# Kernel optimization log

Measured on AMD Instinct MI355X. Metric: run time of the kernel, lower is better.

The kernel has to match this reference:

```python
import jax, jax.numpy as jnp
import numpy as np

IN_CH = 10
OUT_CH = 11
EPS = 1e-5  # torch LayerNorm default


def setup_inputs() -> dict:
    key = jax.random.key(0)
    k_x, k_w = jax.random.split(key, 2)
    N = 8192
    x = jax.random.normal(k_x, (N, IN_CH), dtype=jnp.float32)
    # torch nn.Linear weight: [out_features=3*OUT_CH, in_features=IN_CH]
    W = jax.random.normal(k_w, (3 * OUT_CH, IN_CH), dtype=jnp.float32) * (IN_CH ** -0.5)
    gamma = jnp.ones((IN_CH,), dtype=jnp.float32)
    beta = jnp.zeros((IN_CH,), dtype=jnp.float32)
    return {"x": x, "gamma": gamma, "beta": beta, "W": W}


def reference(x, gamma, beta, W):
    # LayerNorm over channel dim
    mu = jnp.mean(x, axis=-1, keepdims=True)
    var = jnp.var(x, axis=-1, keepdims=True)
    h = (x - mu) / jnp.sqrt(var + EPS) * gamma + beta  # [N, IN_CH]
    # Linear (no bias): x @ W.T -> [N, 3*OUT_CH]
    h = h @ W.T
    # chunk along dim=1 (channel dim for 2D input)
    q, k, v = jnp.split(h, 3, axis=1)  # each [N, OUT_CH]
    scale = IN_CH ** -0.5  # note: scale uses in_channels, per source
    q = q * scale
    sim = jnp.einsum('id,jd->ij', q, k)  # [N, N]
    sim = sim - jax.lax.stop_gradient(jnp.max(sim, axis=-1, keepdims=True))
    attn = jax.nn.softmax(sim, axis=-1)
    out = jnp.einsum('ij,jd->id', attn, v)  # [N, OUT_CH]
    return out
```

## Files before the change

### kernel.cpp

```cpp
#include <hip/hip_runtime.h>

#define NROWS 8192
#define INCH 10
#define NQKV 33
#define OUTCH 11
#define SPLIT 16
#define KB 512
#define QBLK 128

typedef short short8 __attribute__((ext_vector_type(8)));
typedef float f32x16 __attribute__((ext_vector_type(16)));
typedef unsigned int uvec4 __attribute__((ext_vector_type(4)));

#define QB_OFF   0
#define KB_OFF   (NROWS * 32)
#define VT_OFF   (2 * NROWS * 32)
#define PART_OFF (3 * NROWS * 32)

#define SWAP32(a, b) asm("v_permlane32_swap_b32 %0, %1" : "+v"(a), "+v"(b))

__device__ inline unsigned short f2bf(float f) {
  unsigned u = __float_as_uint(f);
  unsigned r = (u + 0x7FFFu + ((u >> 16) & 1u)) >> 16;
  return (unsigned short)r;
}

__global__ __launch_bounds__(128) void qkv_ln_kernel(
    const float* __restrict__ x, const float* __restrict__ gamma,
    const float* __restrict__ beta, const float* __restrict__ W,
    char* __restrict__ ws) {
  __shared__ float sW[NQKV * INCH];
  __shared__ float sg[INCH];
  __shared__ float sb[INCH];
  int tid = threadIdx.x;
  for (int i = tid; i < NQKV * INCH; i += 128) sW[i] = W[i];
  if (tid < INCH) { sg[tid] = gamma[tid]; sb[tid] = beta[tid]; }
  __syncthreads();

  int row = blockIdx.x * 128 + tid;
  const float2* x2 = (const float2*)x;
  float xv[INCH];
#pragma unroll
  for (int j = 0; j < 5; ++j) {
    float2 t = x2[row * 5 + j];
    xv[2 * j] = t.x;
    xv[2 * j + 1] = t.y;
  }

  float mu = 0.f;
#pragma unroll
  for (int i = 0; i < INCH; ++i) mu += xv[i];
  mu *= (1.0f / INCH);
  float var = 0.f;
#pragma unroll
  for (int i = 0; i < INCH; ++i) { float d = xv[i] - mu; var += d * d; }
  var *= (1.0f / INCH);
  float rstd = rsqrtf(var + 1e-5f);
  float h[INCH];
#pragma unroll
  for (int i = 0; i < INCH; ++i) h[i] = (xv[i] - mu) * rstd * sg[i] + sb[i];

  float acc[NQKV];
#pragma unroll
  for (int oc = 0; oc < NQKV; ++oc) {
    float s = 0.f;
#pragma unroll
    for (int i = 0; i < INCH; ++i) s += h[i] * sW[oc * INCH + i];
    acc[oc] = s;
  }

  const float QSC = 0.31622776601683794f * 1.4426950408889634f;

  unsigned short e[16];
  unsigned qw[8];
#pragma unroll
  for (int i = 0; i < 16; ++i) e[i] = (i < OUTCH) ? f2bf(acc[i] * QSC) : 0;
#pragma unroll
  for (int i = 0; i < 8; ++i)
    qw[i] = (unsigned)e[2 * i] | ((unsigned)e[2 * i + 1] << 16);
  uint4* Qb = (uint4*)(ws + QB_OFF);
  Qb[row * 2 + 0] = make_uint4(qw[0], qw[1], qw[2], qw[3]);
  Qb[row * 2 + 1] = make_uint4(qw[4], qw[5], qw[6], qw[7]);
#pragma unroll
  for (int i = 0; i < 16; ++i) e[i] = (i < OUTCH) ? f2bf(acc[OUTCH + i]) : 0;
#pragma unroll
  for (int i = 0; i < 8; ++i)
    qw[i] = (unsigned)e[2 * i] | ((unsigned)e[2 * i + 1] << 16);
  uint4* Kb = (uint4*)(ws + KB_OFF);
  Kb[row * 2 + 0] = make_uint4(qw[0], qw[1], qw[2], qw[3]);
  Kb[row * 2 + 1] = make_uint4(qw[4], qw[5], qw[6], qw[7]);
  unsigned short* VTu = (unsigned short*)(ws + VT_OFF);
  int u0 = (row >> 3) * 16;
  int slot = row & 7;
#pragma unroll
  for (int d = 0; d < 16; ++d) {
    unsigned short v;
    if (d < OUTCH)       v = f2bf(acc[2 * OUTCH + d]);
    else if (d == OUTCH) v = 0x3F80;
    else                 v = 0;
    VTu[(u0 + d) * 8 + slot] = v;
  }
}

__global__ __launch_bounds__(256) void attn_kernel(const char* __restrict__ ws,
                                                   float* __restrict__ part) {
  __shared__ uint4 sK[KB * 2];
  __shared__ uint4 sVT[KB * 2];

  const int tid = threadIdx.x;
  const int lane = tid & 63;
  const int wv = tid >> 6;
  const int h = lane >> 5;
  const int l31 = lane & 31;
  const int qc = blockIdx.x >> 4;
  const int kc = blockIdx.x & 15;
  const int kt0 = kc * KB;
  const int q0 = qc * QBLK + wv * 32;

  const uint4* Qb = (const uint4*)(ws + QB_OFF);
  const uint4* gK = (const uint4*)(ws + KB_OFF) + kt0 * 2;
  const uint4* gV = (const uint4*)(ws + VT_OFF) + kt0 * 2;

#pragma unroll
  for (int i = 0; i < 4; ++i) {
    int o = wv * 64 + 256 * i;
    __builtin_amdgcn_global_load_lds(
        (const __attribute__((address_space(1))) void*)(gK + o + lane),
        (__attribute__((address_space(3))) void*)(sK + o), 16, 0, 0);
    __builtin_amdgcn_global_load_lds(
        (const __attribute__((address_space(1))) void*)(gV + o + lane),
        (__attribute__((address_space(3))) void*)(sVT + o), 16, 0, 0);
  }

  short8 qf = *(const short8*)((const char*)Qb + (q0 + l31) * 32 + h * 16);

  f32x16 oacc;
#pragma unroll
  for (int r = 0; r < 16; ++r) oacc[r] = 0.f;
  f32x16 zf;
#pragma unroll
  for (int r = 0; r < 16; ++r) zf[r] = 0.f;

  __syncthreads();

  for (int it = 0; it < KB / 32; ++it) {
    short8 kf = *(const short8*)((const char*)sK + it * 1024 + l31 * 32 + h * 16);
    f32x16 s = __builtin_amdgcn_mfma_f32_32x32x16_bf16(kf, qf, zf, 0, 0, 0);

    float p[16];
#pragma unroll
    for (int r = 0; r < 16; ++r) p[r] = __builtin_amdgcn_exp2f(s[r]);

#define PK(a, b) __builtin_amdgcn_perm(__float_as_uint(b), __float_as_uint(a), 0x07060302u)
    unsigned P01 = PK(p[0], p[1]), P23 = PK(p[2], p[3]);
    unsigned P45 = PK(p[4], p[5]), P67 = PK(p[6], p[7]);
    unsigned P89 = PK(p[8], p[9]), Pab = PK(p[10], p[11]);
    unsigned Pcd = PK(p[12], p[13]), Pef = PK(p[14], p[15]);
#undef PK
    SWAP32(P01, P45);
    SWAP32(P23, P67);
    SWAP32(P89, Pcd);
    SWAP32(Pab, Pef);

    uvec4 c0 = {P01, P23, P45, P67};
    uvec4 c1 = {P89, Pab, Pcd, Pef};
    short8 a0 = __builtin_bit_cast(short8, c0);
    short8 a1 = __builtin_bit_cast(short8, c1);

    const char* vb = (const char*)sVT;
    short8 v0 = *(const short8*)(vb + (it * 4 + h) * 256 + (lane & 15) * 16);
    short8 v1 = *(const short8*)(vb + (it * 4 + 2 + h) * 256 + (lane & 15) * 16);

    oacc = __builtin_amdgcn_mfma_f32_32x32x16_bf16(a0, v0, oacc, 0, 0, 0);
    oacc = __builtin_amdgcn_mfma_f32_32x32x16_bf16(a1, v1, oacc, 0, 0, 0);
  }

  if (l31 < 12) {
#pragma unroll
    for (int r = 0; r < 16; ++r) {
      int q = (r & 3) + 8 * (r >> 2) + 4 * h;
      part[((size_t)kc * NROWS + q0 + q) * 12 + l31] = oacc[r];
    }
  }
}

__global__ __launch_bounds__(128) void norm_kernel(const float* __restrict__ part,
                                                   float* __restrict__ out) {
  int row = blockIdx.x * 128 + threadIdx.x;
  const float4* p4 = (const float4*)part;
  float r[12];
#pragma unroll
  for (int d = 0; d < 12; ++d) r[d] = 0.f;
#pragma unroll
  for (int kc = 0; kc < SPLIT; ++kc) {
    size_t b = ((size_t)kc * NROWS + row) * 3;
    float4 t0 = p4[b], t1 = p4[b + 1], t2 = p4[b + 2];
    r[0] += t0.x; r[1] += t0.y; r[2] += t0.z; r[3] += t0.w;
    r[4] += t1.x; r[5] += t1.y; r[6] += t1.z; r[7] += t1.w;
    r[8] += t2.x; r[9] += t2.y; r[10] += t2.z; r[11] += t2.w;
  }
  float inv = 1.0f / r[11];
  float* o = out + (size_t)row * OUTCH;
#pragma unroll
  for (int d = 0; d < OUTCH; ++d) o[d] = r[d] * inv;
}

extern "C" void kernel_launch(void* const* d_in, const int* in_sizes, int n_in,
                              void* d_out, int out_size, void* d_ws, size_t ws_size,
                              hipStream_t stream) {
  const float* x = (const float*)d_in[0];
  const float* gamma = (const float*)d_in[1];
  const float* beta = (const float*)d_in[2];
  const float* W = (const float*)d_in[3];
  char* ws = (char*)d_ws;
  float* out = (float*)d_out;
  float* part = (float*)(ws + PART_OFF);

  qkv_ln_kernel<<<NROWS / 128, 128, 0, stream>>>(x, gamma, beta, W, ws);
  attn_kernel<<<(NROWS / QBLK) * SPLIT, 256, 0, stream>>>(ws, part);
  norm_kernel<<<NROWS / 128, 128, 0, stream>>>(part, out);
}
```

Baseline: 25.91 us.

## Process two query tiles per wave to reuse K loads and split K layout

Each wave now handles 64 query rows (two 32-row MFMA tiles) against the same K fragment, doubling QBLK to 256 and halving the attention grid. K is stored as two planar halves (first and second 16 bytes of each row separately), so LDS reads of K become contiguous per half-wave. The pre- and post-processing kernels move to 64-thread blocks, giving more blocks. The intent is to amortize K/V LDS reads and staging across more queries and add MFMA-level ILP, at the cost of more registers and fewer attention blocks (512 instead of 1024), which may reduce occupancy or load balance.

Result: slower. 27.77 us (+7.2%).

```diff
diff --git a/kernel.cpp b/kernel.cpp
--- a/kernel.cpp
+++ b/kernel.cpp
@@ -6,7 +6,7 @@
 #define OUTCH 11
 #define SPLIT 16
 #define KB 512
-#define QBLK 128
+#define QBLK 256
 
 typedef short short8 __attribute__((ext_vector_type(8)));
 typedef float f32x16 __attribute__((ext_vector_type(16)));
@@ -25,7 +25,7 @@
   return (unsigned short)r;
 }
 
-__global__ __launch_bounds__(128) void qkv_ln_kernel(
+__global__ __launch_bounds__(64) void qkv_ln_kernel(
     const float* __restrict__ x, const float* __restrict__ gamma,
     const float* __restrict__ beta, const float* __restrict__ W,
     char* __restrict__ ws) {
@@ -33,11 +33,11 @@
   __shared__ float sg[INCH];
   __shared__ float sb[INCH];
   int tid = threadIdx.x;
-  for (int i = tid; i < NQKV * INCH; i += 128) sW[i] = W[i];
+  for (int i = tid; i < NQKV * INCH; i += 64) sW[i] = W[i];
   if (tid < INCH) { sg[tid] = gamma[tid]; sb[tid] = beta[tid]; }
   __syncthreads();
 
-  int row = blockIdx.x * 128 + tid;
+  int row = blockIdx.x * 64 + tid;
   const float2* x2 = (const float2*)x;
   float xv[INCH];
 #pragma unroll
@@ -87,8 +87,8 @@
   for (int i = 0; i < 8; ++i)
     qw[i] = (unsigned)e[2 * i] | ((unsigned)e[2 * i + 1] << 16);
   uint4* Kb = (uint4*)(ws + KB_OFF);
-  Kb[row * 2 + 0] = make_uint4(qw[0], qw[1], qw[2], qw[3]);
-  Kb[row * 2 + 1] = make_uint4(qw[4], qw[5], qw[6], qw[7]);
+  Kb[row] = make_uint4(qw[0], qw[1], qw[2], qw[3]);
+  Kb[NROWS + row] = make_uint4(qw[4], qw[5], qw[6], qw[7]);
   unsigned short* VTu = (unsigned short*)(ws + VT_OFF);
   int u0 = (row >> 3) * 16;
   int slot = row & 7;
@@ -104,7 +104,7 @@
 
 __global__ __launch_bounds__(256) void attn_kernel(const char* __restrict__ ws,
                                                    float* __restrict__ part) {
-  __shared__ uint4 sK[KB * 2];
+  __shared__ uint4 sK[2 * KB];
   __shared__ uint4 sVT[KB * 2];
 
   const int tid = threadIdx.x;
@@ -115,78 +115,94 @@
   const int qc = blockIdx.x >> 4;
   const int kc = blockIdx.x & 15;
   const int kt0 = kc * KB;
-  const int q0 = qc * QBLK + wv * 32;
-
-  const uint4* Qb = (const uint4*)(ws + QB_OFF);
-  const uint4* gK = (const uint4*)(ws + KB_OFF) + kt0 * 2;
+  const int q0 = qc * QBLK + wv * 64;
+
+  const uint4* gK = (const uint4*)(ws + KB_OFF);
   const uint4* gV = (const uint4*)(ws + VT_OFF) + kt0 * 2;
 
+#pragma unroll
+  for (int c = 0; c < 2; ++c) {
+#pragma unroll
+    for (int i = 0; i < 2; ++i) {
+      int o = wv * 64 + 256 * i;
+      __builtin_amdgcn_global_load_lds(
+          (const __attribute__((address_space(1))) void*)(gK + c * NROWS + kt0 + o + lane),
+          (__attribute__((address_space(3))) void*)(sK + c * KB + o), 16, 0, 0);
+    }
+  }
 #pragma unroll
   for (int i = 0; i < 4; ++i) {
     int o = wv * 64 + 256 * i;
     __builtin_amdgcn_global_load_lds(
-        (const __attribute__((address_space(1))) void*)(gK + o + lane),
-        (__attribute__((address_space(3))) void*)(sK + o), 16, 0, 0);
-    __builtin_amdgcn_global_load_lds(
         (const __attribute__((address_space(1))) void*)(gV + o + lane),
         (__attribute__((address_space(3))) void*)(sVT + o), 16, 0, 0);
   }
 
-  short8 qf = *(const short8*)((const char*)Qb + (q0 + l31) * 32 + h * 16);
-
-  f32x16 oacc;
-#pragma unroll
-  for (int r = 0; r < 16; ++r) oacc[r] = 0.f;
-  f32x16 zf;
-#pragma unroll
-  for (int r = 0; r < 16; ++r) zf[r] = 0.f;
+  const char* Qb = ws + QB_OFF;
+  short8 qf0 = *(const short8*)(Qb + (q0 + l31) * 32 + h * 16);
+  short8 qf1 = *(const short8*)(Qb + (q0 + 32 + l31) * 32 + h * 16);
+
+  f32x16 oacc0, oacc1, zf;
+#pragma unroll
+  for (int r = 0; r < 16; ++r) { oacc0[r] = 0.f; oacc1[r] = 0.f; zf[r] = 0.f; }
 
   __syncthreads();
 
   for (int it = 0; it < KB / 32; ++it) {
-    short8 kf = *(const short8*)((const char*)sK + it * 1024 + l31 * 32 + h * 16);
-    f32x16 s = __builtin_amdgcn_mfma_f32_32x32x16_bf16(kf, qf, zf, 0, 0, 0);
-
-    float p[16];
-#pragma unroll
-    for (int r = 0; r < 16; ++r) p[r] = __builtin_amdgcn_exp2f(s[r]);
-
-#define PK(a, b) __builtin_amdgcn_perm(__float_as_uint(b), __float_as_uint(a), 0x07060302u)
-    unsigned P01 = PK(p[0], p[1]), P23 = PK(p[2], p[3]);
-    unsigned P45 = PK(p[4], p[5]), P67 = PK(p[6], p[7]);
-    unsigned P89 = PK(p[8], p[9]), Pab = PK(p[10], p[11]);
-    unsigned Pcd = PK(p[12], p[13]), Pef = PK(p[14], p[15]);
-#undef PK
-    SWAP32(P01, P45);
-    SWAP32(P23, P67);
-    SWAP32(P89, Pcd);
-    SWAP32(Pab, Pef);
-
-    uvec4 c0 = {P01, P23, P45, P67};
-    uvec4 c1 = {P89, Pab, Pcd, Pef};
-    short8 a0 = __builtin_bit_cast(short8, c0);
-    short8 a1 = __builtin_bit_cast(short8, c1);
+    short8 kf = *(const short8*)((const char*)sK + h * (KB * 16) +
+                                 (it * 32 + l31) * 16);
+    f32x16 s0 = __builtin_amdgcn_mfma_f32_32x32x16_bf16(kf, qf0, zf, 0, 0, 0);
+    f32x16 s1 = __builtin_amdgcn_mfma_f32_32x32x16_bf16(kf, qf1, zf, 0, 0, 0);
 
     const char* vb = (const char*)sVT;
     short8 v0 = *(const short8*)(vb + (it * 4 + h) * 256 + (lane & 15) * 16);
     short8 v1 = *(const short8*)(vb + (it * 4 + 2 + h) * 256 + (lane & 15) * 16);
 
-    oacc = __builtin_amdgcn_mfma_f32_32x32x16_bf16(a0, v0, oacc, 0, 0, 0);
-    oacc = __builtin_amdgcn_mfma_f32_32x32x16_bf16(a1, v1, oacc, 0, 0, 0);
+#define PK(a, b) __builtin_amdgcn_perm(__float_as_uint(b), __float_as_uint(a), 0x07060302u)
+#define MKFRAG(sv, A0, A1)                                                   \
+  {                                                                          \
+    float p[16];                                                             \
+    _Pragma("unroll") for (int r = 0; r < 16; ++r)                           \
+        p[r] = __builtin_amdgcn_exp2f(sv[r]);                                \
+    unsigned P01 = PK(p[0], p[1]), P23 = PK(p[2], p[3]);                     \
+    unsigned P45 = PK(p[4], p[5]), P67 = PK(p[6], p[7]);                     \
+    unsigned P89 = PK(p[8], p[9]), Pab = PK(p[10], p[11]);                   \
+    unsigned Pcd = PK(p[12], p[13]), Pef = PK(p[14], p[15]);                 \
+    SWAP32(P01, P45);                                                        \
+    SWAP32(P23, P67);                                                        \
+    SWAP32(P89, Pcd);                                                        \
+    SWAP32(Pab, Pef);                                                        \
+    uvec4 c0 = {P01, P23, P45, P67};                                         \
+    uvec4 c1 = {P89, Pab, Pcd, Pef};                                         \
+    A0 = __builtin_bit_cast(short8, c0);                                     \
+    A1 = __builtin_bit_cast(short8, c1);                                     \
+  }
+
+    short8 a00, a01, a10, a11;
+    MKFRAG(s0, a00, a01)
+    MKFRAG(s1, a10, a11)
+#undef MKFRAG
+#undef PK
+
+    oacc0 = __builtin_amdgcn_mfma_f32_32x32x16_bf16(a00, v0, oacc0, 0, 0, 0);
+    oacc0 = __builtin_amdgcn_mfma_f32_32x32x16_bf16(a01, v1, oacc0, 0, 0, 0);
+    oacc1 = __builtin_amdgcn_mfma_f32_32x32x16_bf16(a10, v0, oacc1, 0, 0, 0);
+    oacc1 = __builtin_amdgcn_mfma_f32_32x32x16_bf16(a11, v1, oacc1, 0, 0, 0);
   }
 
   if (l31 < 12) {
 #pragma unroll
     for (int r = 0; r < 16; ++r) {
       int q = (r & 3) + 8 * (r >> 2) + 4 * h;
-      part[((size_t)kc * NROWS + q0 + q) * 12 + l31] = oacc[r];
+      part[((size_t)kc * NROWS + q0 + q) * 12 + l31] = oacc0[r];
+      part[((size_t)kc * NROWS + q0 + 32 + q) * 12 + l31] = oacc1[r];
     }
   }
 }
 
-__global__ __launch_bounds__(128) void norm_kernel(const float* __restrict__ part,
-                                                   float* __restrict__ out) {
-  int row = blockIdx.x * 128 + threadIdx.x;
+__global__ __launch_bounds__(64) void norm_kernel(const float* __restrict__ part,
+                                                  float* __restrict__ out) {
+  int row = blockIdx.x * 64 + threadIdx.x;
   const float4* p4 = (const float4*)part;
   float r[12];
 #pragma unroll
@@ -216,7 +232,7 @@
   float* out = (float*)d_out;
   float* part = (float*)(ws + PART_OFF);
 
-  qkv_ln_kernel<<<NROWS / 128, 128, 0, stream>>>(x, gamma, beta, W, ws);
+  qkv_ln_kernel<<<NROWS / 64, 64, 0, stream>>>(x, gamma, beta, W, ws);
   attn_kernel<<<(NROWS / QBLK) * SPLIT, 256, 0, stream>>>(ws, part);
-  norm_kernel<<<NROWS / 128, 128, 0, stream>>>(part, out);
-}
+  norm_kernel<<<NROWS / 64, 64, 0, stream>>>(part, out);
+}
```

## Fuse LayerNorm and QKV projection into attention kernel, recomputing K/V per block

Applied to the files above, without the earlier changes.

Removes the separate QKV/LayerNorm kernel. Each attention block now recomputes LayerNorm and the projection for its 512 key rows and 128 query rows and writes K, V-transposed and Q straight into shared memory. This saves one kernel launch and the global round trip for Q/K/V. In exchange there is redundant work: K/V for each key chunk are recomputed by all 64 query blocks, and the layout of K in shared memory changes. The norm kernel block size also drops to 64 threads.

Measured after the change: 31.89 us. +23.1%, slower.

```diff
diff --git a/kernel.cpp b/kernel.cpp
--- a/kernel.cpp
+++ b/kernel.cpp
@@ -12,10 +12,6 @@
 typedef float f32x16 __attribute__((ext_vector_type(16)));
 typedef unsigned int uvec4 __attribute__((ext_vector_type(4)));
 
-#define QB_OFF   0
-#define KB_OFF   (NROWS * 32)
-#define VT_OFF   (2 * NROWS * 32)
-#define PART_OFF (3 * NROWS * 32)
 
 #define SWAP32(a, b) asm("v_permlane32_swap_b32 %0, %1" : "+v"(a), "+v"(b))
 
@@ -25,87 +21,16 @@
   return (unsigned short)r;
 }
 
-__global__ __launch_bounds__(128) void qkv_ln_kernel(
+__global__ __launch_bounds__(256) void fused_attn_kernel(
     const float* __restrict__ x, const float* __restrict__ gamma,
     const float* __restrict__ beta, const float* __restrict__ W,
-    char* __restrict__ ws) {
+    float* __restrict__ part) {
+  __shared__ uint4 sK[2 * KB];
+  __shared__ uint4 sVT[(KB / 8) * 16];
+  __shared__ uint4 sQ[QBLK * 2];
   __shared__ float sW[NQKV * INCH];
   __shared__ float sg[INCH];
   __shared__ float sb[INCH];
-  int tid = threadIdx.x;
-  for (int i = tid; i < NQKV * INCH; i += 128) sW[i] = W[i];
-  if (tid < INCH) { sg[tid] = gamma[tid]; sb[tid] = beta[tid]; }
-  __syncthreads();
-
-  int row = blockIdx.x * 128 + tid;
-  const float2* x2 = (const float2*)x;
-  float xv[INCH];
-#pragma unroll
-  for (int j = 0; j < 5; ++j) {
-    float2 t = x2[row * 5 + j];
-    xv[2 * j] = t.x;
-    xv[2 * j + 1] = t.y;
-  }
-
-  float mu = 0.f;
-#pragma unroll
-  for (int i = 0; i < INCH; ++i) mu += xv[i];
-  mu *= (1.0f / INCH);
-  float var = 0.f;
-#pragma unroll
-  for (int i = 0; i < INCH; ++i) { float d = xv[i] - mu; var += d * d; }
-  var *= (1.0f / INCH);
-  float rstd = rsqrtf(var + 1e-5f);
-  float h[INCH];
-#pragma unroll
-  for (int i = 0; i < INCH; ++i) h[i] = (xv[i] - mu) * rstd * sg[i] + sb[i];
-
-  float acc[NQKV];
-#pragma unroll
-  for (int oc = 0; oc < NQKV; ++oc) {
-    float s = 0.f;
-#pragma unroll
-    for (int i = 0; i < INCH; ++i) s += h[i] * sW[oc * INCH + i];
-    acc[oc] = s;
-  }
-
-  const float QSC = 0.31622776601683794f * 1.4426950408889634f;
-
-  unsigned short e[16];
-  unsigned qw[8];
-#pragma unroll
-  for (int i = 0; i < 16; ++i) e[i] = (i < OUTCH) ? f2bf(acc[i] * QSC) : 0;
-#pragma unroll
-  for (int i = 0; i < 8; ++i)
-    qw[i] = (unsigned)e[2 * i] | ((unsigned)e[2 * i + 1] << 16);
-  uint4* Qb = (uint4*)(ws + QB_OFF);
-  Qb[row * 2 + 0] = make_uint4(qw[0], qw[1], qw[2], qw[3]);
-  Qb[row * 2 + 1] = make_uint4(qw[4], qw[5], qw[6], qw[7]);
-#pragma unroll
-  for (int i = 0; i < 16; ++i) e[i] = (i < OUTCH) ? f2bf(acc[OUTCH + i]) : 0;
-#pragma unroll
-  for (int i = 0; i < 8; ++i)
-    qw[i] = (unsigned)e[2 * i] | ((unsigned)e[2 * i + 1] << 16);
-  uint4* Kb = (uint4*)(ws + KB_OFF);
-  Kb[row * 2 + 0] = make_uint4(qw[0], qw[1], qw[2], qw[3]);
-  Kb[row * 2 + 1] = make_uint4(qw[4], qw[5], qw[6], qw[7]);
-  unsigned short* VTu = (unsigned short*)(ws + VT_OFF);
-  int u0 = (row >> 3) * 16;
-  int slot = row & 7;
-#pragma unroll
-  for (int d = 0; d < 16; ++d) {
-    unsigned short v;
-    if (d < OUTCH)       v = f2bf(acc[2 * OUTCH + d]);
-    else if (d == OUTCH) v = 0x3F80;
-    else                 v = 0;
-    VTu[(u0 + d) * 8 + slot] = v;
-  }
-}
-
-__global__ __launch_bounds__(256) void attn_kernel(const char* __restrict__ ws,
-                                                   float* __restrict__ part) {
-  __shared__ uint4 sK[KB * 2];
-  __shared__ uint4 sVT[KB * 2];
 
   const int tid = threadIdx.x;
   const int lane = tid & 63;
@@ -115,36 +40,107 @@
   const int qc = blockIdx.x >> 4;
   const int kc = blockIdx.x & 15;
   const int kt0 = kc * KB;
-  const int q0 = qc * QBLK + wv * 32;
-
-  const uint4* Qb = (const uint4*)(ws + QB_OFF);
-  const uint4* gK = (const uint4*)(ws + KB_OFF) + kt0 * 2;
-  const uint4* gV = (const uint4*)(ws + VT_OFF) + kt0 * 2;
-
-#pragma unroll
-  for (int i = 0; i < 4; ++i) {
-    int o = wv * 64 + 256 * i;
-    __builtin_amdgcn_global_load_lds(
-        (const __attribute__((address_space(1))) void*)(gK + o + lane),
-        (__attribute__((address_space(3))) void*)(sK + o), 16, 0, 0);
-    __builtin_amdgcn_global_load_lds(
-        (const __attribute__((address_space(1))) void*)(gV + o + lane),
-        (__attribute__((address_space(3))) void*)(sVT + o), 16, 0, 0);
-  }
-
-  short8 qf = *(const short8*)((const char*)Qb + (q0 + l31) * 32 + h * 16);
-
-  f32x16 oacc;
-#pragma unroll
-  for (int r = 0; r < 16; ++r) oacc[r] = 0.f;
-  f32x16 zf;
-#pragma unroll
-  for (int r = 0; r < 16; ++r) zf[r] = 0.f;
-
+  const int q0blk = qc * QBLK;
+  const int q0 = q0blk + wv * 32;
+
+  for (int i = tid; i < NQKV * INCH; i += 256) sW[i] = W[i];
+  if (tid < INCH) { sg[tid] = gamma[tid]; sb[tid] = beta[tid]; }
   __syncthreads();
 
+  const float2* x2 = (const float2*)x;
+  const float QSC = 0.31622776601683794f * 1.4426950408889634f;
+
+#define LNROW(row, hh)                                                     \
+  {                                                                        \
+    float xv[INCH];                                                        \
+    _Pragma("unroll") for (int j = 0; j < 5; ++j) {                        \
+      float2 t = x2[(row) * 5 + j];                                        \
+      xv[2 * j] = t.x;                                                     \
+      xv[2 * j + 1] = t.y;                                                 \
+    }                                                                      \
+    float mu = 0.f;                                                        \
+    _Pragma("unroll") for (int i = 0; i < INCH; ++i) mu += xv[i];          \
+    mu *= (1.0f / INCH);                                                   \
+    float var = 0.f;                                                       \
+    _Pragma("unroll") for (int i = 0; i < INCH; ++i) {                     \
+      float d = xv[i] - mu;                                                \
+      var += d * d;                                                        \
+    }                                                                      \
+    var *= (1.0f / INCH);                                                  \
+    float rstd = rsqrtf(var + 1e-5f);                                      \
+    _Pragma("unroll") for (int i = 0; i < INCH; ++i)                       \
+        hh[i] = (xv[i] - mu) * rstd * sg[i] + sb[i];                       \
+  }
+
+#pragma unroll
+  for (int i = 0; i < 2; ++i) {
+    int r = tid + 256 * i;
+    int row = kt0 + r;
+    float hv[INCH];
+    LNROW(row, hv)
+    float acc[NQKV - OUTCH];
+#pragma unroll
+    for (int oc = 0; oc < NQKV - OUTCH; ++oc) {
+      float s = 0.f;
+#pragma unroll
+      for (int j = 0; j < INCH; ++j) s += hv[j] * sW[(OUTCH + oc) * INCH + j];
+      acc[oc] = s;
+    }
+    unsigned short e[16];
+#pragma unroll
+    for (int j = 0; j < 16; ++j) e[j] = (j < OUTCH) ? f2bf(acc[j]) : 0;
+    unsigned qw[8];
+#pragma unroll
+    for (int j = 0; j < 8; ++j)
+      qw[j] = (unsigned)e[2 * j] | ((unsigned)e[2 * j + 1] << 16);
+    sK[r] = uint4{qw[0], qw[1], qw[2], qw[3]};
+    sK[KB + r] = uint4{qw[4], qw[5], qw[6], qw[7]};
+    unsigned short* vtu = (unsigned short*)sVT;
+    int u0 = (r >> 3) * 16;
+    int slot = r & 7;
+#pragma unroll
+    for (int d = 0; d < 16; ++d) {
+      unsigned short v;
+      if (d < OUTCH)       v = f2bf(acc[OUTCH + d]);
+      else if (d == OUTCH) v = 0x3F80;
+      else                 v = 0;
+      vtu[(u0 + d) * 8 + slot] = v;
+    }
+  }
+  if (tid < QBLK) {
+    int row = q0blk + tid;
+    float hv[INCH];
+    LNROW(row, hv)
+    unsigned short e[16];
+#pragma unroll
+    for (int oc = 0; oc < 16; ++oc) {
+      float s = 0.f;
+      if (oc < OUTCH) {
+#pragma unroll
+        for (int j = 0; j < INCH; ++j) s += hv[j] * sW[oc * INCH + j];
+      }
+      e[oc] = (oc < OUTCH) ? f2bf(s * QSC) : 0;
+    }
+    unsigned qw[8];
+#pragma unroll
+    for (int j = 0; j < 8; ++j)
+      qw[j] = (unsigned)e[2 * j] | ((unsigned)e[2 * j + 1] << 16);
+    sQ[tid * 2 + 0] = uint4{qw[0], qw[1], qw[2], qw[3]};
+    sQ[tid * 2 + 1] = uint4{qw[4], qw[5], qw[6], qw[7]};
+  }
+#undef LNROW
+
+  __syncthreads();
+
+  short8 qf = *(const short8*)((const char*)sQ + (wv * 32 + l31) * 32 + h * 16);
+
+  f32x16 oacc, zf;
+#pragma unroll
+  for (int r = 0; r < 16; ++r) { oacc[r] = 0.f; zf[r] = 0.f; }
+
   for (int it = 0; it < KB / 32; ++it) {
-    short8 kf = *(const short8*)((const char*)sK + it * 1024 + l31 * 32 + h * 16);
+    short8 kf = *(const short8*)((const char*)sK + h * (KB * 16) +
+                                 (it * 32 + l31) * 16);
     f32x16 s = __builtin_amdgcn_mfma_f32_32x32x16_bf16(kf, qf, zf, 0, 0, 0);
 
     float p[16];
@@ -161,7 +157,6 @@
     SWAP32(P23, P67);
     SWAP32(P89, Pcd);
     SWAP32(Pab, Pef);
-
     uvec4 c0 = {P01, P23, P45, P67};
     uvec4 c1 = {P89, Pab, Pcd, Pef};
     short8 a0 = __builtin_bit_cast(short8, c0);
@@ -184,9 +179,9 @@
   }
 }
 
-__global__ __launch_bounds__(128) void norm_kernel(const float* __restrict__ part,
-                                                   float* __restrict__ out) {
-  int row = blockIdx.x * 128 + threadIdx.x;
+__global__ __launch_bounds__(64) void norm_kernel(const float* __restrict__ part,
+                                                  float* __restrict__ out) {
+  int row = blockIdx.x * 64 + threadIdx.x;
   const float4* p4 = (const float4*)part;
   float r[12];
 #pragma unroll
@@ -212,11 +207,10 @@
   const float* gamma = (const float*)d_in[1];
   const float* beta = (const float*)d_in[2];
   const float* W = (const float*)d_in[3];
-  char* ws = (char*)d_ws;
+  float* part = (float*)d_ws;
   float* out = (float*)d_out;
-  float* part = (float*)(ws + PART_OFF);
-
-  qkv_ln_kernel<<<NROWS / 128, 128, 0, stream>>>(x, gamma, beta, W, ws);
-  attn_kernel<<<(NROWS / QBLK) * SPLIT, 256, 0, stream>>>(ws, part);
-  norm_kernel<<<NROWS / 128, 128, 0, stream>>>(part, out);
-}
+
+  fused_attn_kernel<<<(NROWS / QBLK) * SPLIT, 256, 0, stream>>>(
+      x, gamma, beta, W, part);
+  norm_kernel<<<NROWS / 64, 64, 0, stream>>>(part, out);
+}
```
